# Kernel optimization log

Measured on AMD Instinct MI355X. Metric: run time of the kernel, lower is better.

Reference implementation:

```python
import jax, jax.numpy as jnp
import numpy as np

NEIGHBORHOOD_SIZE = 3
EPS_NORM = 1e-8   # torch CosineSimilarity eps
EPS_DEN = 1e-6


def setup_inputs() -> dict:
    key = jax.random.key(0)
    k1, k2 = jax.random.split(key)
    B, T, C = 8, 2048, 128
    x = jax.random.normal(k1, (B, T, C), dtype=jnp.float32)
    mapping = jnp.sort(jax.random.randint(k2, (B, T), 0, 64), axis=-1).astype(jnp.int64)
    return {"x": x, "mapping": mapping}


def reference(x, mapping):
    B, T, C = x.shape
    # Normalize once, then a single GEMM gives all pairwise cosine sims
    # (avoids the naive B x T x T x C broadcast).
    norms = jnp.linalg.norm(x, axis=-1, keepdims=True)          # [B,T,1]
    xn = x / jnp.maximum(norms, EPS_NORM)
    cos_pred = jnp.einsum('btc,bsc->bts', xn, xn)               # [B,T,T]

    m1 = mapping[:, :, None]                                    # [B,T,1]
    m2 = mapping[:, None, :]                                    # [B,1,T]
    cos_target = (m1 == m2).astype(cos_pred.dtype)              # [B,T,T]

    triu = jnp.triu(jnp.ones((T, T), dtype=bool), k=1)[None]    # strict upper triangle
    neighbor = jnp.abs(m1 - m2) <= NEIGHBORHOOD_SIZE
    padding = (m1 != 0) & (m2 != 0)
    mask = triu & neighbor & padding                             # [B,T,T]

    pred = jnp.where(mask, cos_pred, 0.0)
    tgt = jnp.where(mask, cos_target, 0.0)
    sq = (pred - tgt) ** 2
    loss = sq.sum() / (mask.astype(cos_pred.dtype).sum() + EPS_DEN)
    return loss
```

## Files before the change

kernel.cpp:

```cpp
#include <hip/hip_runtime.h>


#define TT 2048
#define CC 128
#define TM 64
#define SLOTS 4

typedef unsigned short ushort_t;
typedef __attribute__((ext_vector_type(8))) short v8s;
typedef __attribute__((ext_vector_type(4))) float v4f;

__device__ __forceinline__ ushort_t f2bf(float f) {
    unsigned u = __float_as_uint(f);
    return (ushort_t)((u + 0x7FFFu + ((u >> 16) & 1u)) >> 16);
}

__global__ void __launch_bounds__(256) k_prep(const float* __restrict__ x,
                                              ushort_t* __restrict__ xnb) {
    const int wave = threadIdx.x >> 6;
    const int lane = threadIdx.x & 63;
    const int row  = blockIdx.x * 4 + wave;
    float2 v = ((const float2*)(x + (size_t)row * CC))[lane];
    float ss = v.x * v.x + v.y * v.y;
    #pragma unroll
    for (int off = 32; off; off >>= 1) ss += __shfl_xor(ss, off);
    const float rn = 1.0f / fmaxf(sqrtf(ss), 1e-8f);
    const unsigned lo = f2bf(v.x * rn), hi = f2bf(v.y * rn);
    ((unsigned*)(xnb + (size_t)row * CC))[lane] = lo | (hi << 16);
}

__global__ void __launch_bounds__(256) k_tile(const ushort_t* __restrict__ xnb,
                                              const int* __restrict__ map,
                                              float* __restrict__ psum,
                                              int* __restrict__ pcnt) {
    __shared__ __align__(16) ushort_t As[TM * CC];
    __shared__ __align__(16) ushort_t Bs[TM * CC];
    __shared__ int mt_s[TM], et_s[TM], ms_s[TM];
    __shared__ float wsum[4];

    const int tile = blockIdx.x;
    const int slot = blockIdx.y;
    const int tid  = threadIdx.x;
    const int lane = tid & 63;
    const int wave = tid >> 6;
    const int b    = tile >> 5;
    const int t0   = (tile & 31) * TM;
    const int* mb  = map + b * TT;
    const ushort_t* xb = xnb + (size_t)(b * TT) * CC;

    if (tid < TM) {
        const int t = t0 + tid;
        const int m = mb[t];
        int e = t;
        if (m != 0) {
            const int key = m + 3;
            int lo = t + 1, hi = TT;
            while (lo < hi) { int mid = (lo + hi) >> 1; if (mb[mid] <= key) lo = mid + 1; else hi = mid; }
            e = lo - 1;
        }
        mt_s[tid] = m; et_s[tid] = e;
    }
    __syncthreads();

    int e = et_s[lane];
    #pragma unroll
    for (int off = 32; off; off >>= 1) e = max(e, __shfl_xor(e, off));
    const int emax = e;

    if (slot == 0 && wave == 0) {
        int c = et_s[lane] - (t0 + lane);
        #pragma unroll
        for (int off = 32; off; off >>= 1) c += __shfl_xor(c, off);
        if (lane == 0) pcnt[tile] = c;
    }

    int s_base = t0 + slot * TM;
    if (s_base > emax) {
        if (tid == 0) psum[tile * SLOTS + slot] = 0.0f;
        return;
    }

    #pragma unroll
    for (int i = 0; i < 4; ++i) {
        const int pbase = wave * 256 + i * 64;
        const int p = pbase + lane;
        const int row = p >> 4;
        const int sl  = (p & 15) ^ (row & 7);
        __builtin_amdgcn_global_load_lds(
            (const __attribute__((address_space(1))) void*)(xb + (size_t)(t0 + row) * CC + sl * 8),
            (__attribute__((address_space(3))) void*)(&As[pbase * 8]), 16, 0, 0);
    }

    const int wr = wave >> 1, wc = wave & 1;
    const int r16 = lane & 15, kgrp = lane >> 4;
    const int rowA0 = wr * 32 + r16, rowA1 = rowA0 + 16;
    const int rowB0 = wc * 32 + r16, rowB1 = rowB0 + 16;

    float lsum = 0.0f;

    for (; s_base <= emax; s_base += SLOTS * TM) {
        #pragma unroll
        for (int i = 0; i < 4; ++i) {
            const int pbase = wave * 256 + i * 64;
            const int p = pbase + lane;
            const int row = p >> 4;
            const int sl  = (p & 15) ^ (row & 7);
            __builtin_amdgcn_global_load_lds(
                (const __attribute__((address_space(1))) void*)(xb + (size_t)(s_base + row) * CC + sl * 8),
                (__attribute__((address_space(3))) void*)(&Bs[pbase * 8]), 16, 0, 0);
        }
        if (tid < TM) ms_s[tid] = mb[s_base + tid];
        __syncthreads();

        v4f acc00 = {0,0,0,0}, acc01 = {0,0,0,0}, acc10 = {0,0,0,0}, acc11 = {0,0,0,0};
        #pragma unroll
        for (int kk = 0; kk < 4; ++kk) {
            const int sl = kk * 4 + kgrp;
            v8s a0 = *(const v8s*)&As[(rowA0 * 16 + (sl ^ (rowA0 & 7))) * 8];
            v8s a1 = *(const v8s*)&As[(rowA1 * 16 + (sl ^ (rowA1 & 7))) * 8];
            v8s b0 = *(const v8s*)&Bs[(rowB0 * 16 + (sl ^ (rowB0 & 7))) * 8];
            v8s b1 = *(const v8s*)&Bs[(rowB1 * 16 + (sl ^ (rowB1 & 7))) * 8];
            acc00 = __builtin_amdgcn_mfma_f32_16x16x32_bf16(a0, b0, acc00, 0, 0, 0);
            acc01 = __builtin_amdgcn_mfma_f32_16x16x32_bf16(a0, b1, acc01, 0, 0, 0);
            acc10 = __builtin_amdgcn_mfma_f32_16x16x32_bf16(a1, b0, acc10, 0, 0, 0);
            acc11 = __builtin_amdgcn_mfma_f32_16x16x32_bf16(a1, b1, acc11, 0, 0, 0);
        }

        #pragma unroll
        for (int fi = 0; fi < 2; ++fi) {
            #pragma unroll
            for (int fj = 0; fj < 2; ++fj) {
                const v4f a = fi == 0 ? (fj == 0 ? acc00 : acc01) : (fj == 0 ? acc10 : acc11);
                const int s_loc = wc * 32 + fj * 16 + r16;
                const int s     = s_base + s_loc;
                const int m_s   = ms_s[s_loc];
                #pragma unroll
                for (int r = 0; r < 4; ++r) {
                    const int t_loc = wr * 32 + fi * 16 + kgrp * 4 + r;
                    const int t     = t0 + t_loc;
                    const int m_t   = mt_s[t_loc];
                    if ((m_t != 0) & (s > t) & (s <= et_s[t_loc])) {
                        const float d = a[r] - (m_s == m_t ? 1.0f : 0.0f);
                        lsum += d * d;
                    }
                }
            }
        }
        __syncthreads();
    }

    #pragma unroll
    for (int off = 32; off; off >>= 1) lsum += __shfl_xor(lsum, off);
    if (lane == 0) wsum[wave] = lsum;
    __syncthreads();
    if (tid == 0) psum[tile * SLOTS + slot] = wsum[0] + wsum[1] + wsum[2] + wsum[3];
}

__global__ void __launch_bounds__(256) k_final(const float* __restrict__ psum,
                                               const int* __restrict__ pcnt,
                                               float* __restrict__ out,
                                               int n_sum, int n_cnt) {
    __shared__ double ssum[256];
    __shared__ long long scnt[256];
    double s = 0.0; long long c = 0;
    for (int i = threadIdx.x; i < n_sum; i += 256) s += (double)psum[i];
    for (int i = threadIdx.x; i < n_cnt; i += 256) c += (long long)pcnt[i];
    ssum[threadIdx.x] = s; scnt[threadIdx.x] = c;
    __syncthreads();
    #pragma unroll
    for (int off = 128; off; off >>= 1) {
        if (threadIdx.x < off) {
            ssum[threadIdx.x] += ssum[threadIdx.x + off];
            scnt[threadIdx.x] += scnt[threadIdx.x + off];
        }
        __syncthreads();
    }
    if (threadIdx.x == 0) out[0] = (float)(ssum[0] / ((double)scnt[0] + 1e-6));
}

extern "C" void kernel_launch(void* const* d_in, const int* in_sizes, int n_in,
                              void* d_out, int out_size, void* d_ws, size_t ws_size,
                              hipStream_t stream) {
    (void)n_in; (void)out_size; (void)ws_size;
    const float* x   = (const float*)d_in[0];
    const int*   map = (const int*)d_in[1];
    float* out = (float*)d_out;

    const int n_rows  = in_sizes[1];
    const int n_tiles = n_rows / TM;

    ushort_t* xnb = (ushort_t*)d_ws;
    float*    ps  = (float*)((char*)d_ws + (size_t)n_rows * CC * 2);
    int*      pc  = (int*)((char*)ps + (size_t)n_tiles * SLOTS * 4);

    k_prep <<<n_rows / 4, 256, 0, stream>>>(x, xnb);
    k_tile <<<dim3(n_tiles, SLOTS), 256, 0, stream>>>(xnb, map, ps, pc);
    k_final<<<1, 256, 0, stream>>>(ps, pc, out, n_tiles * SLOTS, n_tiles);
}
```

Baseline: 19.84 us.

## Fuse row normalization and bf16 conversion into tile kernel, drop prep launch

Removes the separate normalization kernel and its bf16 workspace round trip. Each tile block now loads fp32 rows directly, computes norms with wave shuffles, and writes swizzled bf16 into LDS for both the A and B tiles. This saves one kernel launch and the intermediate global write and read. In exchange, rows are normalized redundantly across blocks and slots, and the async global-to-LDS loads become synchronous register loads with compute.

```diff
diff --git a/kernel.cpp b/kernel.cpp
--- a/kernel.cpp
+++ b/kernel.cpp
@@ -10,26 +10,14 @@
 typedef __attribute__((ext_vector_type(8))) short v8s;
 typedef __attribute__((ext_vector_type(4))) float v4f;
 
-__device__ __forceinline__ ushort_t f2bf(float f) {
-    unsigned u = __float_as_uint(f);
-    return (ushort_t)((u + 0x7FFFu + ((u >> 16) & 1u)) >> 16);
+__device__ __forceinline__ unsigned pack2bf(float a, float b) {
+    unsigned ua = __float_as_uint(a), ub = __float_as_uint(b);
+    ua = (ua + 0x7FFFu + ((ua >> 16) & 1u)) >> 16;
+    ub = (ub + 0x7FFFu + ((ub >> 16) & 1u)) & 0xFFFF0000u;
+    return ua | ub;
 }
 
-__global__ void __launch_bounds__(256) k_prep(const float* __restrict__ x,
-                                              ushort_t* __restrict__ xnb) {
-    const int wave = threadIdx.x >> 6;
-    const int lane = threadIdx.x & 63;
-    const int row  = blockIdx.x * 4 + wave;
-    float2 v = ((const float2*)(x + (size_t)row * CC))[lane];
-    float ss = v.x * v.x + v.y * v.y;
-    #pragma unroll
-    for (int off = 32; off; off >>= 1) ss += __shfl_xor(ss, off);
-    const float rn = 1.0f / fmaxf(sqrtf(ss), 1e-8f);
-    const unsigned lo = f2bf(v.x * rn), hi = f2bf(v.y * rn);
-    ((unsigned*)(xnb + (size_t)row * CC))[lane] = lo | (hi << 16);
-}
-
-__global__ void __launch_bounds__(256) k_tile(const ushort_t* __restrict__ xnb,
+__global__ void __launch_bounds__(256) k_tile(const float* __restrict__ x,
                                               const int* __restrict__ map,
                                               float* __restrict__ psum,
                                               int* __restrict__ pcnt) {
@@ -46,7 +34,7 @@
     const int b    = tile >> 5;
     const int t0   = (tile & 31) * TM;
     const int* mb  = map + b * TT;
-    const ushort_t* xb = xnb + (size_t)(b * TT) * CC;
+    const float* xg = x + (size_t)(b * TT) * CC;
 
     if (tid < TM) {
         const int t = t0 + tid;
@@ -80,15 +68,16 @@
         return;
     }
 
-    #pragma unroll
-    for (int i = 0; i < 4; ++i) {
-        const int pbase = wave * 256 + i * 64;
-        const int p = pbase + lane;
-        const int row = p >> 4;
-        const int sl  = (p & 15) ^ (row & 7);
-        __builtin_amdgcn_global_load_lds(
-            (const __attribute__((address_space(1))) void*)(xb + (size_t)(t0 + row) * CC + sl * 8),
-            (__attribute__((address_space(3))) void*)(&As[pbase * 8]), 16, 0, 0);
+    #pragma unroll 4
+    for (int i = 0; i < 16; ++i) {
+        const int r = wave * 16 + i;
+        float2 v = ((const float2*)(xg + (size_t)(t0 + r) * CC))[lane];
+        float ss = v.x * v.x + v.y * v.y;
+        #pragma unroll
+        for (int off = 32; off; off >>= 1) ss += __shfl_xor(ss, off);
+        const float rn = 1.0f / fmaxf(sqrtf(ss), 1e-8f);
+        ((unsigned*)&As[(r * 16 + ((lane >> 2) ^ (r & 7))) * 8])[lane & 3] =
+            pack2bf(v.x * rn, v.y * rn);
     }
 
     const int wr = wave >> 1, wc = wave & 1;
@@ -99,15 +88,16 @@
     float lsum = 0.0f;
 
     for (; s_base <= emax; s_base += SLOTS * TM) {
-        #pragma unroll
-        for (int i = 0; i < 4; ++i) {
-            const int pbase = wave * 256 + i * 64;
-            const int p = pbase + lane;
-            const int row = p >> 4;
-            const int sl  = (p & 15) ^ (row & 7);
-            __builtin_amdgcn_global_load_lds(
-                (const __attribute__((address_space(1))) void*)(xb + (size_t)(s_base + row) * CC + sl * 8),
-                (__attribute__((address_space(3))) void*)(&Bs[pbase * 8]), 16, 0, 0);
+        #pragma unroll 4
+        for (int i = 0; i < 16; ++i) {
+            const int r = wave * 16 + i;
+            float2 v = ((const float2*)(xg + (size_t)(s_base + r) * CC))[lane];
+            float ss = v.x * v.x + v.y * v.y;
+            #pragma unroll
+            for (int off = 32; off; off >>= 1) ss += __shfl_xor(ss, off);
+            const float rn = 1.0f / fmaxf(sqrtf(ss), 1e-8f);
+            ((unsigned*)&Bs[(r * 16 + ((lane >> 2) ^ (r & 7))) * 8])[lane & 3] =
+                pack2bf(v.x * rn, v.y * rn);
         }
         if (tid < TM) ms_s[tid] = mb[s_base + tid];
         __syncthreads();
@@ -189,11 +179,9 @@
     const int n_rows  = in_sizes[1];
     const int n_tiles = n_rows / TM;
 
-    ushort_t* xnb = (ushort_t*)d_ws;
-    float*    ps  = (float*)((char*)d_ws + (size_t)n_rows * CC * 2);
-    int*      pc  = (int*)((char*)ps + (size_t)n_tiles * SLOTS * 4);
+    float* ps = (float*)d_ws;
+    int*   pc = (int*)((char*)ps + (size_t)n_tiles * SLOTS * 4);
 
-    k_prep <<<n_rows / 4, 256, 0, stream>>>(x, xnb);
-    k_tile <<<dim3(n_tiles, SLOTS), 256, 0, stream>>>(xnb, map, ps, pc);
+    k_tile <<<dim3(n_tiles, SLOTS), 256, 0, stream>>>(x, map, ps, pc);
     k_final<<<1, 256, 0, stream>>>(ps, pc, out, n_tiles * SLOTS, n_tiles);
 }
```

After: 25.52 us. 1.29x slower.

## Replace per-row binary search with last-index table and prefetch first B tile

Applied to the files above, without the earlier changes.

The prep kernel now also builds a per-batch table giving, for each mapping value, the last position holding it, so the tile kernel reads the neighbourhood end with one lookup instead of a binary search over the mapping. The first A and B tile loads are issued before the metadata work so the global-to-LDS transfer overlaps with it, and a loop barrier is restructured. Tile counts become hard-coded constants, which ties the kernel to the test shape. Blocks that would exit early now still issue their B loads, adding some wasted memory traffic.

```diff
diff --git a/kernel.cpp b/kernel.cpp
--- a/kernel.cpp
+++ b/kernel.cpp
@@ -5,6 +5,10 @@
 #define CC 128
 #define TM 64
 #define SLOTS 4
+#define NTILES 256
+#define TOTAL_BLK (NTILES * SLOTS)
+#define NORM_BLKS 4096
+#define TBL_BLKS 64
 
 typedef unsigned short ushort_t;
 typedef __attribute__((ext_vector_type(8))) short v8s;
@@ -16,21 +20,35 @@
 }
 
 __global__ void __launch_bounds__(256) k_prep(const float* __restrict__ x,
-                                              ushort_t* __restrict__ xnb) {
-    const int wave = threadIdx.x >> 6;
-    const int lane = threadIdx.x & 63;
-    const int row  = blockIdx.x * 4 + wave;
-    float2 v = ((const float2*)(x + (size_t)row * CC))[lane];
-    float ss = v.x * v.x + v.y * v.y;
-    #pragma unroll
-    for (int off = 32; off; off >>= 1) ss += __shfl_xor(ss, off);
-    const float rn = 1.0f / fmaxf(sqrtf(ss), 1e-8f);
-    const unsigned lo = f2bf(v.x * rn), hi = f2bf(v.y * rn);
-    ((unsigned*)(xnb + (size_t)row * CC))[lane] = lo | (hi << 16);
+                                              const int* __restrict__ map,
+                                              ushort_t* __restrict__ xnb,
+                                              int* __restrict__ last_tbl) {
+    const int bid = blockIdx.x;
+    const int tid = threadIdx.x;
+
+    if (bid < NORM_BLKS) {
+        const int wave = tid >> 6, lane = tid & 63;
+        const int row  = bid * 4 + wave;
+        float2 v = ((const float2*)(x + (size_t)row * CC))[lane];
+        float ss = v.x * v.x + v.y * v.y;
+        #pragma unroll
+        for (int off = 32; off; off >>= 1) ss += __shfl_xor(ss, off);
+        const float rn = 1.0f / fmaxf(sqrtf(ss), 1e-8f);
+        const unsigned lo = f2bf(v.x * rn), hi = f2bf(v.y * rn);
+        ((unsigned*)(xnb + (size_t)row * CC))[lane] = lo | (hi << 16);
+    } else {
+        const int row = (bid - NORM_BLKS) * 256 + tid;
+        const int b   = row >> 11, t = row & (TT - 1);
+        const int* mb = map + b * TT;
+        const int m   = mb[t];
+        const int mn  = (t == TT - 1) ? 64 : mb[t + 1];
+        for (int v = m; v < mn; ++v) last_tbl[b * 64 + v] = t;
+    }
 }
 
 __global__ void __launch_bounds__(256) k_tile(const ushort_t* __restrict__ xnb,
                                               const int* __restrict__ map,
+                                              const int* __restrict__ last_tbl,
                                               float* __restrict__ psum,
                                               int* __restrict__ pcnt) {
     __shared__ __align__(16) ushort_t As[TM * CC];
@@ -48,37 +66,7 @@
     const int* mb  = map + b * TT;
     const ushort_t* xb = xnb + (size_t)(b * TT) * CC;
 
-    if (tid < TM) {
-        const int t = t0 + tid;
-        const int m = mb[t];
-        int e = t;
-        if (m != 0) {
-            const int key = m + 3;
-            int lo = t + 1, hi = TT;
-            while (lo < hi) { int mid = (lo + hi) >> 1; if (mb[mid] <= key) lo = mid + 1; else hi = mid; }
-            e = lo - 1;
-        }
-        mt_s[tid] = m; et_s[tid] = e;
-    }
-    __syncthreads();
-
-    int e = et_s[lane];
-    #pragma unroll
-    for (int off = 32; off; off >>= 1) e = max(e, __shfl_xor(e, off));
-    const int emax = e;
-
-    if (slot == 0 && wave == 0) {
-        int c = et_s[lane] - (t0 + lane);
-        #pragma unroll
-        for (int off = 32; off; off >>= 1) c += __shfl_xor(c, off);
-        if (lane == 0) pcnt[tile] = c;
-    }
-
     int s_base = t0 + slot * TM;
-    if (s_base > emax) {
-        if (tid == 0) psum[tile * SLOTS + slot] = 0.0f;
-        return;
-    }
 
     #pragma unroll
     for (int i = 0; i < 4; ++i) {
@@ -89,6 +77,37 @@
         __builtin_amdgcn_global_load_lds(
             (const __attribute__((address_space(1))) void*)(xb + (size_t)(t0 + row) * CC + sl * 8),
             (__attribute__((address_space(3))) void*)(&As[pbase * 8]), 16, 0, 0);
+        const int srow = min(s_base + row, TT - 1);
+        __builtin_amdgcn_global_load_lds(
+            (const __attribute__((address_space(1))) void*)(xb + (size_t)srow * CC + sl * 8),
+            (__attribute__((address_space(3))) void*)(&Bs[pbase * 8]), 16, 0, 0);
+    }
+
+    if (tid < TM) {
+        const int t = t0 + tid;
+        const int m = mb[t];
+        int e = t;
+        if (m != 0) e = last_tbl[b * 64 + min(m + 3, 63)];
+        mt_s[tid] = m; et_s[tid] = e;
+        ms_s[tid] = mb[min(s_base + tid, TT - 1)];
+    }
+    __syncthreads();
+
+    int e = et_s[lane];
+    #pragma unroll
+    for (int off = 32; off; off >>= 1) e = max(e, __shfl_xor(e, off));
+    const int emax = e;
+
+    if (slot == 0 && wave == 0) {
+        int c = et_s[lane] - (t0 + lane);
+        #pragma unroll
+        for (int off = 32; off; off >>= 1) c += __shfl_xor(c, off);
+        if (lane == 0) pcnt[tile] = c;
+    }
+
+    if (s_base > emax) {
+        if (tid == 0) psum[tile * SLOTS + slot] = 0.0f;
+        return;
     }
 
     const int wr = wave >> 1, wc = wave & 1;
@@ -97,20 +116,25 @@
     const int rowB0 = wc * 32 + r16, rowB1 = rowB0 + 16;
 
     float lsum = 0.0f;
+    bool first = true;
 
     for (; s_base <= emax; s_base += SLOTS * TM) {
-        #pragma unroll
-        for (int i = 0; i < 4; ++i) {
-            const int pbase = wave * 256 + i * 64;
-            const int p = pbase + lane;
-            const int row = p >> 4;
-            const int sl  = (p & 15) ^ (row & 7);
-            __builtin_amdgcn_global_load_lds(
-                (const __attribute__((address_space(1))) void*)(xb + (size_t)(s_base + row) * CC + sl * 8),
-                (__attribute__((address_space(3))) void*)(&Bs[pbase * 8]), 16, 0, 0);
-        }
-        if (tid < TM) ms_s[tid] = mb[s_base + tid];
-        __syncthreads();
+        if (!first) {
+            __syncthreads();
+            #pragma unroll
+            for (int i = 0; i < 4; ++i) {
+                const int pbase = wave * 256 + i * 64;
+                const int p = pbase + lane;
+                const int row = p >> 4;
+                const int sl  = (p & 15) ^ (row & 7);
+                __builtin_amdgcn_global_load_lds(
+                    (const __attribute__((address_space(1))) void*)(xb + (size_t)(s_base + row) * CC + sl * 8),
+                    (__attribute__((address_space(3))) void*)(&Bs[pbase * 8]), 16, 0, 0);
+            }
+            if (tid < TM) ms_s[tid] = mb[s_base + tid];
+            __syncthreads();
+        }
+        first = false;
 
         v4f acc00 = {0,0,0,0}, acc01 = {0,0,0,0}, acc10 = {0,0,0,0}, acc11 = {0,0,0,0};
         #pragma unroll
@@ -146,7 +170,6 @@
                 }
             }
         }
-        __syncthreads();
     }
 
     #pragma unroll
@@ -186,14 +209,15 @@
     const int*   map = (const int*)d_in[1];
     float* out = (float*)d_out;
 
-    const int n_rows  = in_sizes[1];
-    const int n_tiles = n_rows / TM;
+    const int n_rows = in_sizes[1];
 
     ushort_t* xnb = (ushort_t*)d_ws;
-    float*    ps  = (float*)((char*)d_ws + (size_t)n_rows * CC * 2);
-    int*      pc  = (int*)((char*)ps + (size_t)n_tiles * SLOTS * 4);
-
-    k_prep <<<n_rows / 4, 256, 0, stream>>>(x, xnb);
-    k_tile <<<dim3(n_tiles, SLOTS), 256, 0, stream>>>(xnb, map, ps, pc);
-    k_final<<<1, 256, 0, stream>>>(ps, pc, out, n_tiles * SLOTS, n_tiles);
-}
+    char*     p   = (char*)d_ws + (size_t)n_rows * CC * 2;
+    int*      tbl = (int*)p;                    p += 8 * 64 * 4;
+    float*    ps  = (float*)p;                  p += (size_t)TOTAL_BLK * 4;
+    int*      pc  = (int*)p;
+
+    k_prep <<<NORM_BLKS + TBL_BLKS, 256, 0, stream>>>(x, map, xnb, tbl);
+    k_tile <<<dim3(NTILES, SLOTS), 256, 0, stream>>>(xnb, map, tbl, ps, pc);
+    k_final<<<1, 256, 0, stream>>>(ps, pc, out, TOTAL_BLK, NTILES);
+}
```

Result: slower. 20.55 us (+3.6%).
